# Kernel optimization log

Hardware: AMD Instinct MI355X
Metric: run time of the kernel (lower is better)

The kernel has to match this reference:

```python
import jax, jax.numpy as jnp
import numpy as np

N_NODES = 50000
N_EDGES = 800000
N_GRAPHS = 256
IN_CH = 128
HID = 128
OUT_CH = 10
BN_EPS = 1e-5


def setup_inputs() -> dict:
    key = jax.random.key(0)
    ks = jax.random.split(key, 32)
    x = jax.random.normal(ks[0], (N_NODES, IN_CH), dtype=jnp.float32)
    edge_index = jax.random.randint(ks[1], (2, N_EDGES), 0, N_NODES)
    batch = jnp.sort(jax.random.randint(ks[2], (N_NODES,), 0, N_GRAPHS))

    def lin(k, fan_in, fan_out):
        return (jax.random.normal(k, (fan_in, fan_out), dtype=jnp.float32)
                * np.float32(1.0 / np.sqrt(fan_in)))

    inp = {"x": x, "edge_index": edge_index, "batch": batch}
    dims = [(IN_CH, HID), (HID, HID), (HID, HID)]
    for i, (fi, fo) in enumerate(dims):
        inp[f"W{i}"] = lin(ks[3 + i], fi, fo)
        inp[f"b{i}"] = jnp.zeros((fo,), jnp.float32)
        inp[f"g{i}"] = jnp.ones((fo,), jnp.float32)
        inp[f"be{i}"] = jnp.zeros((fo,), jnp.float32)
    inp["lin1_w"] = lin(ks[10], 2 * HID, HID)
    inp["lin1_b"] = jnp.zeros((HID,), jnp.float32)
    inp["lin2_w"] = lin(ks[11], HID, OUT_CH)
    inp["lin2_b"] = jnp.zeros((OUT_CH,), jnp.float32)
    return inp


def _gcn_conv(x, W, b, src, dst):
    # PyG GCNConv: h = X W; add self-loops; symmetric D^-1/2 (A+I) D^-1/2 aggregation.
    h = x @ W  # [N, F]
    loops = jnp.arange(N_NODES)
    s = jnp.concatenate([src, loops])
    d = jnp.concatenate([dst, loops])
    deg = jax.ops.segment_sum(jnp.ones_like(d, jnp.float32), d, num_segments=N_NODES)
    dinv = jnp.where(deg > 0, jax.lax.rsqrt(deg), 0.0)
    coef = dinv[s] * dinv[d]  # [E+N]
    out = jax.ops.segment_sum(h[s] * coef[:, None], d, num_segments=N_NODES)
    return out + b


def _batch_norm(x, gamma, beta):
    mean = x.mean(axis=0)
    var = x.var(axis=0)
    return (x - mean) * jax.lax.rsqrt(var + BN_EPS) * gamma + beta


def _forward(x, edge_index, batch,
             W0, b0, g0, be0, W1, b1, g1, be1, W2, b2, g2, be2,
             lin1_w, lin1_b, lin2_w, lin2_b):
    src, dst = edge_index[0], edge_index[1]
    for W, b, g, be in ((W0, b0, g0, be0), (W1, b1, g1, be1), (W2, b2, g2, be2)):
        x = _gcn_conv(x, W, b, src, dst)
        x = jax.nn.relu(_batch_norm(x, g, be))
    x_sum = jax.ops.segment_sum(x, batch, num_segments=N_GRAPHS)  # [G, H]
    counts = jax.ops.segment_sum(jnp.ones((N_NODES,), jnp.float32), batch,
                                 num_segments=N_GRAPHS)
    x_mean = x_sum / jnp.maximum(counts, 1.0)[:, None]
    h = jnp.concatenate([x_mean, x_sum], axis=1)  # [G, 2H]
    h = jax.nn.relu(h @ lin1_w + lin1_b)
    return h @ lin2_w + lin2_b  # [G, OUT_CH]


def reference(x, edge_index, batch,
              W0, b0, g0, be0, W1, b1, g1, be1, W2, b2, g2, be2,
              lin1_w, lin1_b, lin2_w, lin2_b):
    return _forward(x, edge_index, batch,
                    W0, b0, g0, be0, W1, b1, g1, be1, W2, b2, g2, be2,
                    lin1_w, lin1_b, lin2_w, lin2_b)
```

## Files before the change

kernel.cpp:

```cpp
#include <hip/hip_runtime.h>

#define N_NODES 50000
#define N_EDGES 800000
#define N_GRAPHS 256
#define HID 128
#define OUT_CH 10
#define BN_EPS 1e-5f

#define NBUCKET 98
#define BCAP 10240

#define OFF_H       0
#define OFF_BNPART  3134464
#define OFF_CSRD    3200000
#define OFF_WBT     4000000
#define OFF_AGG     6400000
#define OFF_ROWPTR  12850000
#define OFF_CSR     12950004
#define OFF_DINV    13750004
#define OFF_BNCOEF  13800004
#define OFF_POOL    13800260
#define OFF_CNT     13833028
#define OFF_BCNT    13833284
#define OFF_BSTART  13833444

#define WBT_PITCH 136

typedef __attribute__((ext_vector_type(8))) short bf16x8;
typedef __attribute__((ext_vector_type(4))) float f32x4;

__device__ __forceinline__ ushort f2bf(float f) {
    union { float f; unsigned u; } v; v.f = f;
    unsigned r = v.u + 0x7FFFu + ((v.u >> 16) & 1u);
    return (ushort)(r >> 16);
}
__device__ __forceinline__ float bf2f(unsigned u16) {
    return __uint_as_float(u16 << 16);
}

__global__ void k_zero(int* bcnt) {
    int i = threadIdx.x;
    if (i < NBUCKET) bcnt[i] = 0;
}

__global__ __launch_bounds__(256) void k_bucket(const int* __restrict__ ei,
                                                int* __restrict__ bcnt,
                                                int2* __restrict__ buf) {
    __shared__ int histL[NBUCKET], baseL[NBUCKET], curL[NBUCKET];
    int t = threadIdx.x;
    if (t < NBUCKET) histL[t] = 0;
    __syncthreads();
    const int stride = gridDim.x * 256;
    for (int i = blockIdx.x * 256 + t; i < N_EDGES; i += stride)
        atomicAdd(&histL[ei[N_EDGES + i] >> 9], 1);
    __syncthreads();
    if (t < NBUCKET) {
        baseL[t] = atomicAdd(&bcnt[t], histL[t]);
        curL[t] = 0;
    }
    __syncthreads();
    for (int i = blockIdx.x * 256 + t; i < N_EDGES; i += stride) {
        int s = ei[i];
        int d = ei[N_EDGES + i];
        int b = d >> 9;
        int p = baseL[b] + atomicAdd(&curL[b], 1);
        if (p < BCAP) buf[b * BCAP + p] = make_int2(s, d);
    }
}

__global__ void k_bscan(const int* __restrict__ bcnt, int* __restrict__ bstart,
                        int* __restrict__ rowptr) {
    if (threadIdx.x == 0) {
        int acc = 0;
        for (int b = 0; b < NBUCKET; ++b) { bstart[b] = acc; acc += bcnt[b]; }
        bstart[NBUCKET] = acc;
        rowptr[N_NODES] = acc;
    }
}

__global__ __launch_bounds__(512) void k_csrbuild(const int2* __restrict__ buf,
                                                  const int* __restrict__ bcnt,
                                                  const int* __restrict__ bstart,
                                                  int* __restrict__ rowptr,
                                                  int* __restrict__ csr,
                                                  float* __restrict__ dinv) {
    __shared__ int off[512];
    __shared__ int cur[512];
    __shared__ int img[BCAP];
    int b = blockIdx.x, t = threadIdx.x;
    int node0 = b << 9;
    int cnt = bcnt[b];
    int ebase = bstart[b];
    const int2* mybuf = buf + b * BCAP;

    off[t] = 0;
    __syncthreads();
    for (int e = t; e < cnt; e += 512)
        atomicAdd(&off[mybuf[e].y - node0], 1);
    __syncthreads();
    int mydeg = off[t];
    for (int o = 1; o < 512; o <<= 1) {
        int x = (t >= o) ? off[t - o] : 0;
        __syncthreads();
        off[t] += x;
        __syncthreads();
    }
    int inc = off[t];
    cur[t] = inc - mydeg;
    int node = node0 + t;
    if (node < N_NODES) {
        rowptr[node] = ebase + inc - mydeg;
        dinv[node] = rsqrtf((float)(mydeg + 1));
    }
    __syncthreads();
    for (int e = t; e < cnt; e += 512) {
        int2 pr = mybuf[e];
        int p = atomicAdd(&cur[pr.y - node0], 1);
        img[p] = pr.x;
    }
    __syncthreads();
    int lo = inc - mydeg;
    for (int i = lo + 1; i < inc; ++i) {
        int key = img[i];
        int j = i - 1;
        while (j >= lo && img[j] > key) { img[j + 1] = img[j]; --j; }
        img[j + 1] = key;
    }
    __syncthreads();
    for (int e = t; e < cnt; e += 512)
        csr[ebase + e] = img[e];
}

__global__ void k_fill(const int* __restrict__ csr, const float* __restrict__ dinv,
                       float* __restrict__ csrd) {
    int i = blockIdx.x * 1024 + threadIdx.x;
    if (i < N_EDGES) csrd[i] = dinv[csr[i]];
}

__global__ void k_wprep(const float* __restrict__ W, ushort* __restrict__ Wbt) {
    int i = blockIdx.x * 256 + threadIdx.x;
    if (i < 16384) {
        int k = i >> 7, c = i & 127;
        Wbt[c * WBT_PITCH + k] = f2bf(W[i]);
    }
}

template <int BN>
__global__ __launch_bounds__(256) void k_gemm(const float* __restrict__ X,
                                              const ushort* __restrict__ Wbt,
                                              ushort* __restrict__ Hb,
                                              const float* __restrict__ coef,
                                              int nrows) {
    __shared__ __align__(16) ushort Wt[128 * WBT_PITCH];
    int t = threadIdx.x;
    for (int i = t; i < 2176; i += 256)
        ((uint4*)Wt)[i] = ((const uint4*)Wbt)[i];
    __syncthreads();

    int wv = t >> 6, l = t & 63;
    int m = l & 15;
    int kg = l >> 4;
    int row = blockIdx.x * 64 + wv * 16 + m;
    bool valid = row < nrows;
    const float* xr = X + (long)row * 128;

    f32x4 acc[8];
#pragma unroll
    for (int n = 0; n < 8; ++n) acc[n] = (f32x4){0.f, 0.f, 0.f, 0.f};

#pragma unroll
    for (int t4 = 0; t4 < 4; ++t4) {
        int k0 = t4 * 32 + kg * 8;
        float xv[8];
        if (valid) {
            float4 u0 = *(const float4*)(xr + k0);
            float4 u1 = *(const float4*)(xr + k0 + 4);
            if (BN) {
                float4 s0 = *(const float4*)(coef + k0);
                float4 s1 = *(const float4*)(coef + k0 + 4);
                float4 h0 = *(const float4*)(coef + 128 + k0);
                float4 h1 = *(const float4*)(coef + 128 + k0 + 4);
                u0.x = fmaxf(u0.x * s0.x + h0.x, 0.f);
                u0.y = fmaxf(u0.y * s0.y + h0.y, 0.f);
                u0.z = fmaxf(u0.z * s0.z + h0.z, 0.f);
                u0.w = fmaxf(u0.w * s0.w + h0.w, 0.f);
                u1.x = fmaxf(u1.x * s1.x + h1.x, 0.f);
                u1.y = fmaxf(u1.y * s1.y + h1.y, 0.f);
                u1.z = fmaxf(u1.z * s1.z + h1.z, 0.f);
                u1.w = fmaxf(u1.w * s1.w + h1.w, 0.f);
            }
            xv[0] = u0.x; xv[1] = u0.y; xv[2] = u0.z; xv[3] = u0.w;
            xv[4] = u1.x; xv[5] = u1.y; xv[6] = u1.z; xv[7] = u1.w;
        } else {
#pragma unroll
            for (int j = 0; j < 8; ++j) xv[j] = 0.f;
        }
        union { ushort u[8]; bf16x8 v; } A;
#pragma unroll
        for (int j = 0; j < 8; ++j) A.u[j] = f2bf(xv[j]);

#pragma unroll
        for (int n = 0; n < 8; ++n) {
            bf16x8 b = *(const bf16x8*)(&Wt[(n * 16 + m) * WBT_PITCH + k0]);
            acc[n] = __builtin_amdgcn_mfma_f32_16x16x32_bf16(A.v, b, acc[n], 0, 0, 0);
        }
    }

    int srow0 = blockIdx.x * 64 + wv * 16 + kg * 4;
#pragma unroll
    for (int n = 0; n < 8; ++n)
#pragma unroll
        for (int r = 0; r < 4; ++r) {
            int rr = srow0 + r;
            if (rr < nrows) Hb[(long)rr * 128 + n * 16 + m] = f2bf(acc[n][r]);
        }
}

__global__ __launch_bounds__(256) void k_agg(const ushort* __restrict__ Hb,
                                             const int* __restrict__ rowptr,
                                             const int* __restrict__ csr,
                                             const float* __restrict__ csrd,
                                             const float* __restrict__ dinv,
                                             const float* __restrict__ bias,
                                             float* __restrict__ OUT) {
    int wave = threadIdx.x >> 6, lane = threadIdx.x & 63;
    int v = blockIdx.x * 4 + wave;
    if (v >= N_NODES) return;
    int half = lane >> 5, qd = lane & 31;
    int c = qd * 4;
    float dv = dinv[v];
    int e0 = rowptr[v];
    int deg = rowptr[v + 1] - e0;
    float a0 = 0.f, a1 = 0.f, a2 = 0.f, a3 = 0.f;

    for (int base = 0; base < deg; base += 64) {
        int mye = base + lane;
        int idx = 0; float dvi = 0.f;
        if (mye < deg) { idx = csr[e0 + mye]; dvi = csrd[e0 + mye]; }
        int n = min(64, deg - base);
        int P = (n + 1) >> 1;
        int p = 0;
#define EDGE(pp) { \
        int sl = 2 * (pp) + half; \
        int s = __shfl(idx, sl); \
        float cf = __shfl(dvi, sl) * dv; \
        uint2 qv = *(const uint2*)(Hb + (long)s * 128 + c); \
        a0 += cf * bf2f(qv.x & 0xFFFFu); \
        a1 += cf * bf2f(qv.x >> 16); \
        a2 += cf * bf2f(qv.y & 0xFFFFu); \
        a3 += cf * bf2f(qv.y >> 16); }
        for (; p + 4 <= P; p += 4) { EDGE(p) EDGE(p + 1) EDGE(p + 2) EDGE(p + 3) }
        for (; p < P; ++p) { EDGE(p) }
#undef EDGE
    }
    a0 += __shfl_xor(a0, 32);
    a1 += __shfl_xor(a1, 32);
    a2 += __shfl_xor(a2, 32);
    a3 += __shfl_xor(a3, 32);
    if (half == 0) {
        uint2 qv = *(const uint2*)(Hb + (long)v * 128 + c);
        float cs = dv * dv;
        float4 bb = *(const float4*)(bias + c);
        float4 o;
        o.x = a0 + cs * bf2f(qv.x & 0xFFFFu) + bb.x;
        o.y = a1 + cs * bf2f(qv.x >> 16) + bb.y;
        o.z = a2 + cs * bf2f(qv.y & 0xFFFFu) + bb.z;
        o.w = a3 + cs * bf2f(qv.y >> 16) + bb.w;
        *(float4*)(OUT + (long)v * 128 + c) = o;
    }
}

__global__ __launch_bounds__(256) void k_bnstats(const float* __restrict__ X,
                                                 float* __restrict__ part) {
    int ch = threadIdx.x & 127;
    int half = threadIdx.x >> 7;
    float s = 0.f, q = 0.f;
    for (int v = blockIdx.x * 2 + half; v < N_NODES; v += 512) {
        float x = X[(long)v * 128 + ch];
        s += x;
        q += x * x;
    }
    __shared__ float sh[256];
    sh[threadIdx.x] = s;
    __syncthreads();
    float s2 = (half == 0) ? s + sh[threadIdx.x + 128] : 0.f;
    __syncthreads();
    sh[threadIdx.x] = q;
    __syncthreads();
    if (half == 0) {
        float q2 = q + sh[threadIdx.x + 128];
        part[blockIdx.x * 256 + ch] = s2;
        part[blockIdx.x * 256 + 128 + ch] = q2;
    }
}

__global__ void k_bnred(const float* __restrict__ part, const float* __restrict__ g,
                        const float* __restrict__ be, float* __restrict__ coef) {
    int t = threadIdx.x;
    int ch = t & 127, stat = t >> 7;
    float acc = 0.f;
    for (int b = 0; b < 256; ++b) acc += part[b * 256 + stat * 128 + ch];
    __shared__ float sh[256];
    sh[t] = acc;
    __syncthreads();
    if (stat == 0) {
        float inv_n = 1.0f / (float)N_NODES;
        float mean = acc * inv_n;
        float var = sh[128 + ch] * inv_n - mean * mean;
        float sc = g[ch] * rsqrtf(var + BN_EPS);
        coef[ch] = sc;
        coef[128 + ch] = be[ch] - mean * sc;
    }
}

__global__ __launch_bounds__(256) void k_pool(const float* __restrict__ X,
                                              const int* __restrict__ batch,
                                              const float* __restrict__ coef,
                                              float* __restrict__ pool,
                                              float* __restrict__ cnt) {
    __shared__ int bounds[2];
    int g = blockIdx.x, t = threadIdx.x;
    if (t < 2) {
        int target = g + t;
        int lo = 0, hi = N_NODES;
        while (lo < hi) {
            int mid = (lo + hi) >> 1;
            if (batch[mid] < target) lo = mid + 1; else hi = mid;
        }
        bounds[t] = lo;
    }
    __syncthreads();
    int start = bounds[0], end = bounds[1];
    int ch = t & 127, half = t >> 7;
    float sc = coef[ch], sh = coef[128 + ch];
    float acc = 0.f;
    for (int v = start + half; v < end; v += 2)
        acc += fmaxf(X[(long)v * 128 + ch] * sc + sh, 0.f);
    __shared__ float red[256];
    red[t] = acc;
    __syncthreads();
    if (half == 0) {
        pool[g * 128 + ch] = red[ch] + red[128 + ch];
        if (ch == 0) cnt[g] = (float)(end - start);
    }
}

__global__ __launch_bounds__(128) void k_mlp(const float* __restrict__ pool,
                                             const float* __restrict__ cnt,
                                             const float* __restrict__ w1,
                                             const float* __restrict__ b1,
                                             const float* __restrict__ w2,
                                             const float* __restrict__ b2,
                                             float* __restrict__ out) {
    __shared__ float h[256];
    __shared__ float h1[128];
    int g = blockIdx.x, t = threadIdx.x;
    float s = pool[g * 128 + t];
    float c = cnt[g];
    h[t] = s / fmaxf(c, 1.0f);
    h[128 + t] = s;
    __syncthreads();
    float acc = b1[t];
#pragma unroll 4
    for (int i = 0; i < 256; ++i) acc += h[i] * w1[i * 128 + t];
    h1[t] = fmaxf(acc, 0.f);
    __syncthreads();
    if (t < OUT_CH) {
        float o = b2[t];
#pragma unroll 4
        for (int j = 0; j < 128; ++j) o += h1[j] * w2[j * OUT_CH + t];
        out[g * OUT_CH + t] = o;
    }
}

extern "C" void kernel_launch(void* const* d_in, const int* in_sizes, int n_in,
                              void* d_out, int out_size, void* d_ws, size_t ws_size,
                              hipStream_t stream) {
    const float* x = (const float*)d_in[0];
    const int* ei = (const int*)d_in[1];
    const int* batch = (const int*)d_in[2];
    const float* W[3] = {(const float*)d_in[3], (const float*)d_in[7], (const float*)d_in[11]};
    const float* b[3] = {(const float*)d_in[4], (const float*)d_in[8], (const float*)d_in[12]};
    const float* gm[3] = {(const float*)d_in[5], (const float*)d_in[9], (const float*)d_in[13]};
    const float* be[3] = {(const float*)d_in[6], (const float*)d_in[10], (const float*)d_in[14]};
    const float* w1 = (const float*)d_in[15];
    const float* b1 = (const float*)d_in[16];
    const float* w2 = (const float*)d_in[17];
    const float* b2 = (const float*)d_in[18];
    float* out = (float*)d_out;

    float* ws = (float*)d_ws;
    ushort* Hb = (ushort*)(ws + OFF_H);
    float* bnpart = ws + OFF_BNPART;
    float* csrd = ws + OFF_CSRD;
    ushort* Wbt = (ushort*)(ws + OFF_WBT);
    float* AGG = ws + OFF_AGG;
    int2* bucketBuf = (int2*)(ws + OFF_AGG);
    int* rowptr = (int*)(ws + OFF_ROWPTR);
    int* csr = (int*)(ws + OFF_CSR);
    float* dinv = ws + OFF_DINV;
    float* bncoef = ws + OFF_BNCOEF;
    float* pool = ws + OFF_POOL;
    float* cnt = ws + OFF_CNT;
    int* bcnt = (int*)(ws + OFF_BCNT);
    int* bstart = (int*)(ws + OFF_BSTART);

    const int nb_node4 = (N_NODES + 3) / 4;

    hipLaunchKernelGGL(k_zero, dim3(1), dim3(128), 0, stream, bcnt);
    hipLaunchKernelGGL(k_bucket, dim3(392), dim3(256), 0, stream, ei, bcnt, bucketBuf);
    hipLaunchKernelGGL(k_bscan, dim3(1), dim3(64), 0, stream, bcnt, bstart, rowptr);
    hipLaunchKernelGGL(k_csrbuild, dim3(NBUCKET), dim3(512), 0, stream,
                       bucketBuf, bcnt, bstart, rowptr, csr, dinv);
    hipLaunchKernelGGL(k_fill, dim3((N_EDGES + 1023) / 1024), dim3(1024), 0, stream,
                       csr, dinv, csrd);
    for (int layer = 0; layer < 3; ++layer)
        hipLaunchKernelGGL(k_wprep, dim3(64), dim3(256), 0, stream,
                           W[layer], Wbt + layer * 128 * WBT_PITCH);

    const int gemm_blocks = (N_NODES + 63) / 64;
    for (int layer = 0; layer < 3; ++layer) {
        const float* cur_x = (layer == 0) ? x : AGG;
        const ushort* wbt_l = Wbt + layer * 128 * WBT_PITCH;
        if (layer == 0) {
            hipLaunchKernelGGL(k_gemm<0>, dim3(gemm_blocks), dim3(256), 0, stream,
                               cur_x, wbt_l, Hb, (const float*)nullptr, N_NODES);
        } else {
            hipLaunchKernelGGL(k_gemm<1>, dim3(gemm_blocks), dim3(256), 0, stream,
                               cur_x, wbt_l, Hb, bncoef, N_NODES);
        }
        hipLaunchKernelGGL(k_agg, dim3(nb_node4), dim3(256), 0, stream,
                           Hb, rowptr, csr, csrd, dinv, b[layer], AGG);
        hipLaunchKernelGGL(k_bnstats, dim3(256), dim3(256), 0, stream, AGG, bnpart);
        hipLaunchKernelGGL(k_bnred, dim3(1), dim3(256), 0, stream,
                           bnpart, gm[layer], be[layer], bncoef);
    }

    hipLaunchKernelGGL(k_pool, dim3(N_GRAPHS), dim3(256), 0, stream,
                       AGG, batch, bncoef, pool, cnt);
    hipLaunchKernelGGL(k_mlp, dim3(N_GRAPHS), dim3(128), 0, stream,
                       pool, cnt, w1, b1, w2, b2, out);
}
```

Baseline: 480.0 us.

## Move CSR segment sort into per-node wave bitonic kernel fused with coef fill

The CSR build no longer stages each bucket in a 40KB shared-memory image and insertion-sorts it with one thread per node. It now scatters neighbor indices straight to global memory. A new kernel assigns one wavefront per node and sorts each adjacency segment with a register bitonic sort over shuffles, falling back to a serial sort for degree above 64. The same kernel writes the dinv-per-edge array, replacing the separate fill kernel. This cuts the LDS footprint so k_csrbuild can get higher occupancy, and it removes the serialized insertion sort, at the cost of extra global traffic for the scatter and re-read.

```diff
diff --git a/kernel.cpp b/kernel.cpp
--- a/kernel.cpp
+++ b/kernel.cpp
@@ -86,7 +86,6 @@
                                                   float* __restrict__ dinv) {
     __shared__ int off[512];
     __shared__ int cur[512];
-    __shared__ int img[BCAP];
     int b = blockIdx.x, t = threadIdx.x;
     int node0 = b << 9;
     int cnt = bcnt[b];
@@ -106,7 +105,7 @@
         __syncthreads();
     }
     int inc = off[t];
-    cur[t] = inc - mydeg;
+    cur[t] = ebase + inc - mydeg;
     int node = node0 + t;
     if (node < N_NODES) {
         rowptr[node] = ebase + inc - mydeg;
@@ -116,25 +115,45 @@
     for (int e = t; e < cnt; e += 512) {
         int2 pr = mybuf[e];
         int p = atomicAdd(&cur[pr.y - node0], 1);
-        img[p] = pr.x;
-    }
-    __syncthreads();
-    int lo = inc - mydeg;
-    for (int i = lo + 1; i < inc; ++i) {
-        int key = img[i];
-        int j = i - 1;
-        while (j >= lo && img[j] > key) { img[j + 1] = img[j]; --j; }
-        img[j + 1] = key;
-    }
-    __syncthreads();
-    for (int e = t; e < cnt; e += 512)
-        csr[ebase + e] = img[e];
-}
-
-__global__ void k_fill(const int* __restrict__ csr, const float* __restrict__ dinv,
-                       float* __restrict__ csrd) {
-    int i = blockIdx.x * 1024 + threadIdx.x;
-    if (i < N_EDGES) csrd[i] = dinv[csr[i]];
+        csr[p] = pr.x;
+    }
+}
+
+__global__ __launch_bounds__(256) void k_sortseg(const int* __restrict__ rowptr,
+                                                 int* __restrict__ csr,
+                                                 const float* __restrict__ dinv,
+                                                 float* __restrict__ csrd) {
+    int wave = threadIdx.x >> 6, lane = threadIdx.x & 63;
+    int v = blockIdx.x * 4 + wave;
+    if (v >= N_NODES) return;
+    int e0 = rowptr[v], deg = rowptr[v + 1] - e0;
+    if (deg <= 64) {
+        int val = (lane < deg) ? csr[e0 + lane] : 0x7FFFFFFF;
+#pragma unroll
+        for (int k = 2; k <= 64; k <<= 1)
+#pragma unroll
+            for (int j = k >> 1; j > 0; j >>= 1) {
+                int other = __shfl_xor(val, j);
+                bool up = ((lane & k) == 0);
+                bool lower = ((lane & j) == 0);
+                int mn = min(val, other), mx = max(val, other);
+                val = (up == lower) ? mn : mx;
+            }
+        if (lane < deg) {
+            csr[e0 + lane] = val;
+            csrd[e0 + lane] = dinv[val];
+        }
+    } else {
+        if (lane == 0) {
+            for (int i = e0 + 1; i < e0 + deg; ++i) {
+                int key = csr[i];
+                int j = i - 1;
+                while (j >= e0 && csr[j] > key) { csr[j + 1] = csr[j]; --j; }
+                csr[j + 1] = key;
+            }
+        }
+        for (int e = e0 + lane; e < e0 + deg; e += 64) csrd[e] = dinv[csr[e]];
+    }
 }
 
 __global__ void k_wprep(const float* __restrict__ W, ushort* __restrict__ Wbt) {
@@ -412,8 +431,8 @@
     hipLaunchKernelGGL(k_bscan, dim3(1), dim3(64), 0, stream, bcnt, bstart, rowptr);
     hipLaunchKernelGGL(k_csrbuild, dim3(NBUCKET), dim3(512), 0, stream,
                        bucketBuf, bcnt, bstart, rowptr, csr, dinv);
-    hipLaunchKernelGGL(k_fill, dim3((N_EDGES + 1023) / 1024), dim3(1024), 0, stream,
-                       csr, dinv, csrd);
+    hipLaunchKernelGGL(k_sortseg, dim3(nb_node4), dim3(256), 0, stream,
+                       rowptr, csr, dinv, csrd);
     for (int layer = 0; layer < 3; ++layer)
         hipLaunchKernelGGL(k_wprep, dim3(64), dim3(256), 0, stream,
                            W[layer], Wbt + layer * 128 * WBT_PITCH);
```

Measured after the change: 449.1 us. 6.4% less time.
